# Optimization experiments

Measured on AMD Instinct MI355X. Metric: run time of the kernel, lower is better.

## Reference

```python
import jax, jax.numpy as jnp
import numpy as np

D_MODEL = 1024
NUM_HEADS = 16
D_K = D_MODEL // NUM_HEADS


def setup_inputs() -> dict:
    key = jax.random.key(0)
    ks = jax.random.split(key, 11)
    B, S, D = 2, 2048, D_MODEL
    s = 1.0 / np.sqrt(D)
    return {
        "Q": jax.random.normal(ks[0], (B, S, D), jnp.float32),
        "K": jax.random.normal(ks[1], (B, S, D), jnp.float32),
        "V": jax.random.normal(ks[2], (B, S, D), jnp.float32),
        "Wq": jax.random.normal(ks[3], (D, D), jnp.float32) * s,
        "bq": jax.random.normal(ks[4], (D,), jnp.float32) * s,
        "Wk": jax.random.normal(ks[5], (D, D), jnp.float32) * s,
        "bk": jax.random.normal(ks[6], (D,), jnp.float32) * s,
        "Wv": jax.random.normal(ks[7], (D, D), jnp.float32) * s,
        "bv": jax.random.normal(ks[8], (D,), jnp.float32) * s,
        "Wo": jax.random.normal(ks[9], (D, D), jnp.float32) * s,
        "bo": jax.random.normal(ks[10], (D,), jnp.float32) * s,
    }


def _split_heads(x):
    B, S, D = x.shape
    return x.reshape(B, S, NUM_HEADS, D_K).transpose(0, 2, 1, 3)  # [B,H,S,d_k]


def reference(Q, K, V, Wq, bq, Wk, bk, Wv, bv, Wo, bo):
    q = _split_heads(Q @ Wq + bq)
    k = _split_heads(K @ Wk + bk)
    v = _split_heads(V @ Wv + bv)
    scale = 1.0 / np.sqrt(D_K)
    scores = jnp.einsum('bhqd,bhkd->bhqk', q, k) * scale
    P = jax.nn.softmax(scores, axis=-1)  # max-subtract + exp + normalize
    O = jnp.einsum('bhqk,bhkd->bhqd', P, v)
    B, H, S, dk = O.shape
    O = O.transpose(0, 2, 1, 3).reshape(B, S, H * dk)
    return O @ Wo + bo
```

## Files before the change

kernel.cpp:

```cpp
#include <hip/hip_runtime.h>
#include <math.h>

#define S_LEN 2048
#define DMODEL 1024
#define NHEADS 16
#define DK 64

#define QSCALE 0.1803368801111244f

typedef __attribute__((ext_vector_type(8))) _Float16 f16x8;
typedef __attribute__((ext_vector_type(2))) __fp16 hf16x2;
typedef __attribute__((ext_vector_type(4))) float f32x4;

static __device__ __forceinline__ unsigned short f2h(float f) {
    _Float16 h = (_Float16)f;
    return __builtin_bit_cast(unsigned short, h);
}

static __device__ __forceinline__ unsigned pack2(float a, float b) {
    hf16x2 h = __builtin_amdgcn_cvt_pkrtz(a, b);
    return __builtin_bit_cast(unsigned, h);
}

static __device__ __forceinline__ void gload16(const void* g, void* l) {
    __builtin_amdgcn_global_load_lds(
        (const __attribute__((address_space(1))) void*)g,
        (__attribute__((address_space(3))) void*)l, 16, 0, 0);
}

__global__ __launch_bounds__(256)
void cvt_f16_kernel(const float* __restrict__ s0, const float* __restrict__ s1,
                    const float* __restrict__ s2, unsigned short* __restrict__ d)
{
    const int z = blockIdx.y;
    const float* src = z == 0 ? s0 : (z == 1 ? s1 : s2);
    unsigned short* dst = d + (size_t)z * 4194304;
    const int i = (blockIdx.x * 256 + threadIdx.x) * 8;
    float4 a = *reinterpret_cast<const float4*>(src + i);
    float4 b = *reinterpret_cast<const float4*>(src + i + 4);
    uint4 o;
    o.x = pack2(a.x, a.y);
    o.y = pack2(a.z, a.w);
    o.z = pack2(b.x, b.y);
    o.w = pack2(b.z, b.w);
    *reinterpret_cast<uint4*>(dst + i) = o;
}

__global__ __launch_bounds__(256)
void wprep_kernel(const float* __restrict__ w0, const float* __restrict__ w1,
                  const float* __restrict__ w2, const float* __restrict__ w3,
                  unsigned short* __restrict__ wt)
{
    __shared__ float tile[64][65];
    const int z = blockIdx.z;
    const float* W = z == 0 ? w0 : (z == 1 ? w1 : (z == 2 ? w2 : w3));
    unsigned short* Wt = wt + (size_t)z * 1048576;
    const int k0 = blockIdx.x * 64, n0 = blockIdx.y * 64;
    const int t = threadIdx.x;
    #pragma unroll
    for (int i = 0; i < 4; ++i) {
        int idx = i * 256 + t;
        int r = idx >> 4, c4 = (idx & 15) * 4;
        float4 v = *reinterpret_cast<const float4*>(W + (size_t)(k0 + r) * 1024 + n0 + c4);
        tile[r][c4 + 0] = v.x; tile[r][c4 + 1] = v.y;
        tile[r][c4 + 2] = v.z; tile[r][c4 + 3] = v.w;
    }
    __syncthreads();
    #pragma unroll
    for (int i = 0; i < 4; ++i) {
        int idx = i * 256 + t;
        int nr = idx >> 4, kc4 = (idx & 15) * 4;
        ushort4 h;
        h.x = f2h(tile[kc4 + 0][nr]); h.y = f2h(tile[kc4 + 1][nr]);
        h.z = f2h(tile[kc4 + 2][nr]); h.w = f2h(tile[kc4 + 3][nr]);
        *reinterpret_cast<ushort4*>(Wt + (size_t)(n0 + nr) * 1024 + k0 + kc4) = h;
    }
}

__global__ __launch_bounds__(512)
void gemm_mfma_kernel(const unsigned short* __restrict__ xh_base,
                      const unsigned short* __restrict__ wt_base,
                      const float* __restrict__ b0, const float* __restrict__ b1,
                      const float* __restrict__ b2,
                      void* __restrict__ dst_base, int mode_base)
{
    __shared__ char Als[16384];
    __shared__ char Bls[16384];

    const int z = blockIdx.z;
    const char* Ag = (const char*)(xh_base + (size_t)z * 4194304);
    const char* Bg = (const char*)(wt_base + (size_t)z * 1048576);
    const float* bias = z == 0 ? b0 : (z == 1 ? b1 : b2);
    const int mode = mode_base < 0 ? z : mode_base;

    const int tid = threadIdx.x;
    const int w = tid >> 6, l = tid & 63, a = l & 15, g = l >> 4;
    const int wm = w >> 2, wn = w & 3;
    const int bm = blockIdx.y * 128, bn = blockIdx.x * 128;

    const int srow = tid >> 3;
    const int sc8 = tid & 7;

    f32x4 acc[4][2] = {};

    for (int k0b = 0; k0b < 2048; k0b += 128) {
        #pragma unroll
        for (int it = 0; it < 2; ++it) {
            const int row = it * 64 + srow;
            const int gc = (sc8 << 4) ^ ((row & 7) << 4);
            gload16(Ag + (size_t)(bm + row) * 2048 + k0b + gc,
                    &Als[(size_t)(it * 512 + tid) * 16]);
            gload16(Bg + (size_t)(bn + row) * 2048 + k0b + gc,
                    &Bls[(size_t)(it * 512 + tid) * 16]);
        }
        __syncthreads();
        #pragma unroll
        for (int kc = 0; kc < 2; ++kc) {
            f16x8 af[4], bf[2];
            #pragma unroll
            for (int mi = 0; mi < 4; ++mi) {
                const int row = wm * 64 + 16 * mi + a;
                af[mi] = *reinterpret_cast<const f16x8*>(
                    &Als[row * 128 + ((kc * 64 + g * 16) ^ ((row & 7) << 4))]);
            }
            #pragma unroll
            for (int ni = 0; ni < 2; ++ni) {
                const int row = wn * 32 + 16 * ni + a;
                bf[ni] = *reinterpret_cast<const f16x8*>(
                    &Bls[row * 128 + ((kc * 64 + g * 16) ^ ((row & 7) << 4))]);
            }
            __builtin_amdgcn_s_setprio(1);
            #pragma unroll
            for (int mi = 0; mi < 4; ++mi)
                #pragma unroll
                for (int ni = 0; ni < 2; ++ni)
                    acc[mi][ni] = __builtin_amdgcn_mfma_f32_16x16x32_f16(
                        af[mi], bf[ni], acc[mi][ni], 0, 0, 0);
            __builtin_amdgcn_s_setprio(0);
        }
        __syncthreads();
    }

    void* mydst = (mode == 3) ? dst_base
                 : (void*)((unsigned short*)dst_base + (size_t)z * 4194304);

    #pragma unroll
    for (int ni = 0; ni < 2; ++ni) {
        const int n = bn + wn * 32 + 16 * ni + a;
        const float bv = bias[n];
        #pragma unroll
        for (int mi = 0; mi < 4; ++mi) {
            const int mbase = bm + wm * 64 + 16 * mi + g * 4;
            if (mode == 3) {
                float* o = (float*)mydst;
                #pragma unroll
                for (int r = 0; r < 4; ++r)
                    o[(size_t)(mbase + r) * 1024 + n] = acc[mi][ni][r] + bv;
            } else if (mode == 2) {
                unsigned short* o = (unsigned short*)mydst;
                const int b = mbase >> 11, s = mbase & (S_LEN - 1);
                const int h = n >> 6, d = n & (DK - 1);
                ushort4 st;
                st.x = f2h(acc[mi][ni][0] + bv);
                st.y = f2h(acc[mi][ni][1] + bv);
                st.z = f2h(acc[mi][ni][2] + bv);
                st.w = f2h(acc[mi][ni][3] + bv);
                *reinterpret_cast<ushort4*>(
                    o + ((size_t)((b * NHEADS + h) * DK + d)) * S_LEN + s) = st;
            } else {
                unsigned short* o = (unsigned short*)mydst;
                const float sc = (mode == 0) ? QSCALE : 1.0f;
                #pragma unroll
                for (int r = 0; r < 4; ++r) {
                    const int m = mbase + r;
                    const int b = m >> 11, s = m & (S_LEN - 1);
                    const int h = n >> 6, d = n & (DK - 1);
                    o[((size_t)((b * NHEADS + h) * S_LEN + s)) * DK + d] =
                        f2h((acc[mi][ni][r] + bv) * sc);
                }
            }
        }
    }
}

__global__ __launch_bounds__(512, 4)
void attn_mfma_kernel(const unsigned short* __restrict__ qb,
                      const unsigned short* __restrict__ kb,
                      const unsigned short* __restrict__ vt,
                      unsigned short* __restrict__ ob)
{
    __shared__ char Kls[2][8192];
    __shared__ char Vls[2][8192];
    __shared__ unsigned short Pl[8][32][72];

    const int tid = threadIdx.x;
    const int w = tid >> 6;
    const int p = w >> 2;
    const int wsub = w & 3;
    const int l = tid & 63;
    const int a = l & 15;
    const int g = l >> 4;
    const int bh = blockIdx.y;
    const int q0 = blockIdx.x * 128 + wsub * 32;

    const unsigned short* qhead = qb + (size_t)bh * S_LEN * DK;
    const char* khead = (const char*)(kb + (size_t)bh * S_LEN * DK);
    const char* vhead = (const char*)(vt + (size_t)bh * DK * S_LEN);

    f16x8 qf[2][2];
    #pragma unroll
    for (int j = 0; j < 2; ++j)
        #pragma unroll
        for (int c = 0; c < 2; ++c)
            qf[j][c] = *reinterpret_cast<const f16x8*>(
                qhead + (size_t)(q0 + 16 * j + a) * DK + 32 * c + 8 * g);

    f16x8 onesf;
    #pragma unroll
    for (int i = 0; i < 8; ++i) onesf[i] = (_Float16)1.f;

    f32x4 oacc[4][2] = {};
    f32x4 lacc[2] = {};
    float mrun[2] = {-INFINITY, -INFINITY};

    const int srow = tid >> 3;
    const int sgc = ((tid & 7) << 4) ^ ((srow & 7) << 4);

    #define STAGE1(t2)                                                          \
        do {                                                                    \
            gload16(khead + (size_t)((t2) * 64 + srow) * 128 + sgc,             \
                    &Kls[(t2) & 1][(size_t)w * 1024]);                          \
            gload16(vhead + (size_t)srow * 4096 + (size_t)(t2) * 128 + sgc,     \
                    &Vls[(t2) & 1][(size_t)w * 1024]);                          \
        } while (0)

    STAGE1(0);
    STAGE1(1);
    __syncthreads();

    for (int i = 0; i < 16; ++i) {
        f16x8 kf[2][4];
        #pragma unroll
        for (int c = 0; c < 2; ++c)
            #pragma unroll
            for (int T = 0; T < 4; ++T) {
                const int row = 16 * T + a;
                kf[c][T] = *reinterpret_cast<const f16x8*>(
                    &Kls[p][row * 128 + ((64 * c + 16 * g) ^ ((row & 7) << 4))]);
            }

        #pragma unroll
        for (int j = 0; j < 2; ++j) {
            f32x4 sacc[4] = {};
            __builtin_amdgcn_s_setprio(1);
            #pragma unroll
            for (int c = 0; c < 2; ++c)
                #pragma unroll
                for (int T = 0; T < 4; ++T)
                    sacc[T] = __builtin_amdgcn_mfma_f32_16x16x32_f16(
                        kf[c][T], qf[j][c], sacc[T], 0, 0, 0);
            __builtin_amdgcn_s_setprio(0);

            float lm = -INFINITY;
            #pragma unroll
            for (int T = 0; T < 4; ++T)
                #pragma unroll
                for (int r = 0; r < 4; ++r) lm = fmaxf(lm, sacc[T][r]);

            if (!__all(lm <= mrun[j] + 8.f)) {
                float vmax = fmaxf(lm, __shfl_xor(lm, 16));
                vmax = fmaxf(vmax, __shfl_xor(vmax, 32));
                const float mnew = fmaxf(mrun[j], vmax);
                const float corr = __builtin_amdgcn_exp2f(mrun[j] - mnew);
                #pragma unroll
                for (int t = 0; t < 4; ++t) {
                    oacc[t][j][0] *= corr; oacc[t][j][1] *= corr;
                    oacc[t][j][2] *= corr; oacc[t][j][3] *= corr;
                }
                lacc[j][0] *= corr; lacc[j][1] *= corr;
                lacc[j][2] *= corr; lacc[j][3] *= corr;
                mrun[j] = mnew;
            }

            const float mj = mrun[j];
            #pragma unroll
            for (int T = 0; T < 4; ++T) {
                float e0 = __builtin_amdgcn_exp2f(sacc[T][0] - mj);
                float e1 = __builtin_amdgcn_exp2f(sacc[T][1] - mj);
                float e2 = __builtin_amdgcn_exp2f(sacc[T][2] - mj);
                float e3 = __builtin_amdgcn_exp2f(sacc[T][3] - mj);
                unsigned* dst = reinterpret_cast<unsigned*>(
                    &Pl[w][16 * j + a][16 * T + 4 * g]);
                dst[0] = pack2(e0, e1);
                dst[1] = pack2(e2, e3);
            }
        }

        f16x8 vf[2][4];
        #pragma unroll
        for (int c = 0; c < 2; ++c)
            #pragma unroll
            for (int t = 0; t < 4; ++t) {
                const int row = 16 * t + a;
                vf[c][t] = *reinterpret_cast<const f16x8*>(
                    &Vls[p][row * 128 + ((64 * c + 16 * g) ^ ((row & 7) << 4))]);
            }

        __syncthreads();
        if (i < 15) {
            STAGE1(2 * i + 2);
            STAGE1(2 * i + 3);
        }

        #pragma unroll
        for (int c = 0; c < 2; ++c) {
            f16x8 pf[2];
            #pragma unroll
            for (int j = 0; j < 2; ++j)
                pf[j] = *reinterpret_cast<const f16x8*>(
                    &Pl[w][16 * j + a][32 * c + 8 * g]);
            __builtin_amdgcn_s_setprio(1);
            #pragma unroll
            for (int t = 0; t < 4; ++t)
                #pragma unroll
                for (int j = 0; j < 2; ++j)
                    oacc[t][j] = __builtin_amdgcn_mfma_f32_16x16x32_f16(
                        vf[c][t], pf[j], oacc[t][j], 0, 0, 0);
            #pragma unroll
            for (int j = 0; j < 2; ++j)
                lacc[j] = __builtin_amdgcn_mfma_f32_16x16x32_f16(
                    onesf, pf[j], lacc[j], 0, 0, 0);
            __builtin_amdgcn_s_setprio(0);
        }
        __syncthreads();
    }
    #undef STAGE1

    float* Ob = (float*)Pl;
    float* Ml = (float*)Kls;
    if (p == 1) {
        #pragma unroll
        for (int j = 0; j < 2; ++j) {
            if (g == 0) {
                Ml[((wsub * 2 + j) * 2 + 0) * 16 + a] = mrun[j];
                Ml[((wsub * 2 + j) * 2 + 1) * 16 + a] = lacc[j][0];
            }
            #pragma unroll
            for (int t = 0; t < 4; ++t)
                #pragma unroll
                for (int r = 0; r < 4; ++r)
                    Ob[((wsub * 2 + j) * 64 + 16 * t + 4 * g + r) * 16 + a] =
                        oacc[t][j][r];
        }
    }
    __syncthreads();
    if (p == 0) {
        const int b = bh >> 4;
        const int h = bh & (NHEADS - 1);
        #pragma unroll
        for (int j = 0; j < 2; ++j) {
            const float m1 = Ml[((wsub * 2 + j) * 2 + 0) * 16 + a];
            const float l1 = Ml[((wsub * 2 + j) * 2 + 1) * 16 + a];
            const float m0 = mrun[j];
            const float ms = fmaxf(m0, m1);
            const float c0 = __builtin_amdgcn_exp2f(m0 - ms);
            const float c1 = __builtin_amdgcn_exp2f(m1 - ms);
            const float inv = 1.f / (lacc[j][0] * c0 + l1 * c1);
            unsigned short* dst0 =
                ob + (size_t)(b * S_LEN + q0 + 16 * j + a) * DMODEL + h * DK;
            #pragma unroll
            for (int t = 0; t < 4; ++t) {
                ushort4 st;
                #pragma unroll
                for (int r = 0; r < 4; ++r) {
                    const float o1 =
                        Ob[((wsub * 2 + j) * 64 + 16 * t + 4 * g + r) * 16 + a];
                    const float val = (oacc[t][j][r] * c0 + o1 * c1) * inv;
                    ((unsigned short*)&st)[r] = f2h(val);
                }
                *reinterpret_cast<ushort4*>(dst0 + 16 * t + 4 * g) = st;
            }
        }
    }
}

extern "C" void kernel_launch(void* const* d_in, const int* in_sizes, int n_in,
                              void* d_out, int out_size, void* d_ws, size_t ws_size,
                              hipStream_t stream)
{
    const float* Q  = (const float*)d_in[0];
    const float* K  = (const float*)d_in[1];
    const float* V  = (const float*)d_in[2];
    const float* Wq = (const float*)d_in[3];
    const float* bq = (const float*)d_in[4];
    const float* Wk = (const float*)d_in[5];
    const float* bk = (const float*)d_in[6];
    const float* Wv = (const float*)d_in[7];
    const float* bv = (const float*)d_in[8];
    const float* Wo = (const float*)d_in[9];
    const float* bo = (const float*)d_in[10];
    float* out = (float*)d_out;

    unsigned short* xh  = (unsigned short*)d_ws;
    unsigned short* wt  = xh + (size_t)3 * 4194304;
    unsigned short* qb  = wt + (size_t)4 * 1048576;
    unsigned short* kb  = qb + 4194304;
    unsigned short* vtb = kb + 4194304;
    unsigned short* obh = vtb + 4194304;

    cvt_f16_kernel<<<dim3(2048, 3), 256, 0, stream>>>(Q, K, V, xh);
    wprep_kernel<<<dim3(16, 16, 4), 256, 0, stream>>>(Wq, Wk, Wv, Wo, wt);

    gemm_mfma_kernel<<<dim3(8, 32, 3), 512, 0, stream>>>(
        xh, wt, bq, bk, bv, qb, -1);

    attn_mfma_kernel<<<dim3(S_LEN / 128, 2 * NHEADS), 512, 0, stream>>>(qb, kb, vtb, obh);

    gemm_mfma_kernel<<<dim3(8, 32, 1), 512, 0, stream>>>(
        obh, wt + (size_t)3 * 1048576, bo, bo, bo, out, 3);
}
```

Baseline: 137.1 us.

## Fuse fp32-to-fp16 input conversion into projection GEMM A-tile loading

Drops the separate cvt_f16 pass over Q/K/V. The projection GEMM now reads fp32 activations directly into registers, packs them to fp16, and writes them into swizzled LDS. This removes one kernel launch and the write plus re-read of a 24 MB fp16 intermediate. In exchange, the A tile is re-read in fp32 by each of the 8 column blocks, doubling A-side global traffic in the GEMM, and the A loads now go through registers instead of async global-to-LDS loads.

```diff
diff --git a/kernel.cpp b/kernel.cpp
--- a/kernel.cpp
+++ b/kernel.cpp
@@ -26,24 +26,6 @@
     __builtin_amdgcn_global_load_lds(
         (const __attribute__((address_space(1))) void*)g,
         (__attribute__((address_space(3))) void*)l, 16, 0, 0);
-}
-
-__global__ __launch_bounds__(256)
-void cvt_f16_kernel(const float* __restrict__ s0, const float* __restrict__ s1,
-                    const float* __restrict__ s2, unsigned short* __restrict__ d)
-{
-    const int z = blockIdx.y;
-    const float* src = z == 0 ? s0 : (z == 1 ? s1 : s2);
-    unsigned short* dst = d + (size_t)z * 4194304;
-    const int i = (blockIdx.x * 256 + threadIdx.x) * 8;
-    float4 a = *reinterpret_cast<const float4*>(src + i);
-    float4 b = *reinterpret_cast<const float4*>(src + i + 4);
-    uint4 o;
-    o.x = pack2(a.x, a.y);
-    o.y = pack2(a.z, a.w);
-    o.z = pack2(b.x, b.y);
-    o.w = pack2(b.z, b.w);
-    *reinterpret_cast<uint4*>(dst + i) = o;
 }
 
 __global__ __launch_bounds__(256)
@@ -78,41 +60,60 @@
 }
 
 __global__ __launch_bounds__(512)
-void gemm_mfma_kernel(const unsigned short* __restrict__ xh_base,
+void proj_gemm_kernel(const float* __restrict__ x0, const float* __restrict__ x1,
+                      const float* __restrict__ x2,
                       const unsigned short* __restrict__ wt_base,
                       const float* __restrict__ b0, const float* __restrict__ b1,
                       const float* __restrict__ b2,
-                      void* __restrict__ dst_base, int mode_base)
+                      unsigned short* __restrict__ dst_base)
 {
     __shared__ char Als[16384];
     __shared__ char Bls[16384];
 
     const int z = blockIdx.z;
-    const char* Ag = (const char*)(xh_base + (size_t)z * 4194304);
+    const float* Ag = z == 0 ? x0 : (z == 1 ? x1 : x2);
     const char* Bg = (const char*)(wt_base + (size_t)z * 1048576);
     const float* bias = z == 0 ? b0 : (z == 1 ? b1 : b2);
-    const int mode = mode_base < 0 ? z : mode_base;
+    const int mode = z;
 
     const int tid = threadIdx.x;
     const int w = tid >> 6, l = tid & 63, a = l & 15, g = l >> 4;
     const int wm = w >> 2, wn = w & 3;
     const int bm = blockIdx.y * 128, bn = blockIdx.x * 128;
 
+    const int arow = tid >> 2;
+    const int ac16 = tid & 3;
+    const int aswz = (arow & 7) << 4;
     const int srow = tid >> 3;
     const int sc8 = tid & 7;
 
     f32x4 acc[4][2] = {};
 
-    for (int k0b = 0; k0b < 2048; k0b += 128) {
+    for (int ks = 0; ks < 16; ++ks) {
+        const float* ap = Ag + (size_t)(bm + arow) * 1024 + ks * 64 + 16 * ac16;
+        float4 a0 = reinterpret_cast<const float4*>(ap)[0];
+        float4 a1 = reinterpret_cast<const float4*>(ap)[1];
+        float4 a2 = reinterpret_cast<const float4*>(ap)[2];
+        float4 a3 = reinterpret_cast<const float4*>(ap)[3];
+
         #pragma unroll
         for (int it = 0; it < 2; ++it) {
             const int row = it * 64 + srow;
             const int gc = (sc8 << 4) ^ ((row & 7) << 4);
-            gload16(Ag + (size_t)(bm + row) * 2048 + k0b + gc,
-                    &Als[(size_t)(it * 512 + tid) * 16]);
-            gload16(Bg + (size_t)(bn + row) * 2048 + k0b + gc,
+            gload16(Bg + (size_t)(bn + row) * 2048 + ks * 128 + gc,
                     &Bls[(size_t)(it * 512 + tid) * 16]);
         }
+
+        uint4 w0, w1;
+        w0.x = pack2(a0.x, a0.y); w0.y = pack2(a0.z, a0.w);
+        w0.z = pack2(a1.x, a1.y); w0.w = pack2(a1.z, a1.w);
+        w1.x = pack2(a2.x, a2.y); w1.y = pack2(a2.z, a2.w);
+        w1.z = pack2(a3.x, a3.y); w1.w = pack2(a3.z, a3.w);
+        const int abase = arow * 128;
+        const int aoff = 32 * ac16;
+        *reinterpret_cast<uint4*>(&Als[abase + (aoff ^ aswz)]) = w0;
+        *reinterpret_cast<uint4*>(&Als[abase + ((aoff + 16) ^ aswz)]) = w1;
+
         __syncthreads();
         #pragma unroll
         for (int kc = 0; kc < 2; ++kc) {
@@ -141,8 +142,7 @@
         __syncthreads();
     }
 
-    void* mydst = (mode == 3) ? dst_base
-                 : (void*)((unsigned short*)dst_base + (size_t)z * 4194304);
+    unsigned short* mydst = dst_base + (size_t)z * 4194304;
 
     #pragma unroll
     for (int ni = 0; ni < 2; ++ni) {
@@ -151,13 +151,7 @@
         #pragma unroll
         for (int mi = 0; mi < 4; ++mi) {
             const int mbase = bm + wm * 64 + 16 * mi + g * 4;
-            if (mode == 3) {
-                float* o = (float*)mydst;
-                #pragma unroll
-                for (int r = 0; r < 4; ++r)
-                    o[(size_t)(mbase + r) * 1024 + n] = acc[mi][ni][r] + bv;
-            } else if (mode == 2) {
-                unsigned short* o = (unsigned short*)mydst;
+            if (mode == 2) {
                 const int b = mbase >> 11, s = mbase & (S_LEN - 1);
                 const int h = n >> 6, d = n & (DK - 1);
                 ushort4 st;
@@ -166,19 +160,91 @@
                 st.z = f2h(acc[mi][ni][2] + bv);
                 st.w = f2h(acc[mi][ni][3] + bv);
                 *reinterpret_cast<ushort4*>(
-                    o + ((size_t)((b * NHEADS + h) * DK + d)) * S_LEN + s) = st;
+                    mydst + ((size_t)((b * NHEADS + h) * DK + d)) * S_LEN + s) = st;
             } else {
-                unsigned short* o = (unsigned short*)mydst;
                 const float sc = (mode == 0) ? QSCALE : 1.0f;
                 #pragma unroll
                 for (int r = 0; r < 4; ++r) {
                     const int m = mbase + r;
                     const int b = m >> 11, s = m & (S_LEN - 1);
                     const int h = n >> 6, d = n & (DK - 1);
-                    o[((size_t)((b * NHEADS + h) * S_LEN + s)) * DK + d] =
+                    mydst[((size_t)((b * NHEADS + h) * S_LEN + s)) * DK + d] =
                         f2h((acc[mi][ni][r] + bv) * sc);
                 }
             }
+        }
+    }
+}
+
+__global__ __launch_bounds__(512)
+void out_gemm_kernel(const unsigned short* __restrict__ Agh,
+                     const unsigned short* __restrict__ Bgh,
+                     const float* __restrict__ bias, float* __restrict__ out)
+{
+    __shared__ char Als[16384];
+    __shared__ char Bls[16384];
+
+    const char* Ag = (const char*)Agh;
+    const char* Bg = (const char*)Bgh;
+
+    const int tid = threadIdx.x;
+    const int w = tid >> 6, l = tid & 63, a = l & 15, g = l >> 4;
+    const int wm = w >> 2, wn = w & 3;
+    const int bm = blockIdx.y * 128, bn = blockIdx.x * 128;
+
+    const int srow = tid >> 3;
+    const int sc8 = tid & 7;
+
+    f32x4 acc[4][2] = {};
+
+    for (int k0b = 0; k0b < 2048; k0b += 128) {
+        #pragma unroll
+        for (int it = 0; it < 2; ++it) {
+            const int row = it * 64 + srow;
+            const int gc = (sc8 << 4) ^ ((row & 7) << 4);
+            gload16(Ag + (size_t)(bm + row) * 2048 + k0b + gc,
+                    &Als[(size_t)(it * 512 + tid) * 16]);
+            gload16(Bg + (size_t)(bn + row) * 2048 + k0b + gc,
+                    &Bls[(size_t)(it * 512 + tid) * 16]);
+        }
+        __syncthreads();
+        #pragma unroll
+        for (int kc = 0; kc < 2; ++kc) {
+            f16x8 af[4], bf[2];
+            #pragma unroll
+            for (int mi = 0; mi < 4; ++mi) {
+                const int row = wm * 64 + 16 * mi + a;
+                af[mi] = *reinterpret_cast<const f16x8*>(
+                    &Als[row * 128 + ((kc * 64 + g * 16) ^ ((row & 7) << 4))]);
+            }
+            #pragma unroll
+            for (int ni = 0; ni < 2; ++ni) {
+                const int row = wn * 32 + 16 * ni + a;
+                bf[ni] = *reinterpret_cast<const f16x8*>(
+                    &Bls[row * 128 + ((kc * 64 + g * 16) ^ ((row & 7) << 4))]);
+            }
+            __builtin_amdgcn_s_setprio(1);
+            #pragma unroll
+            for (int mi = 0; mi < 4; ++mi)
+                #pragma unroll
+                for (int ni = 0; ni < 2; ++ni)
+                    acc[mi][ni] = __builtin_amdgcn_mfma_f32_16x16x32_f16(
+                        af[mi], bf[ni], acc[mi][ni], 0, 0, 0);
+            __builtin_amdgcn_s_setprio(0);
+        }
+        __syncthreads();
+    }
+
+    #pragma unroll
+    for (int ni = 0; ni < 2; ++ni) {
+        const int n = bn + wn * 32 + 16 * ni + a;
+        const float bv = bias[n];
+        #pragma unroll
+        for (int mi = 0; mi < 4; ++mi) {
+            const int mbase = bm + wm * 64 + 16 * mi + g * 4;
+            #pragma unroll
+            for (int r = 0; r < 4; ++r)
+                out[(size_t)(mbase + r) * 1024 + n] = acc[mi][ni][r] + bv;
         }
     }
 }
@@ -408,14 +474,13 @@
     unsigned short* vtb = kb + 4194304;
     unsigned short* obh = vtb + 4194304;
 
-    cvt_f16_kernel<<<dim3(2048, 3), 256, 0, stream>>>(Q, K, V, xh);
     wprep_kernel<<<dim3(16, 16, 4), 256, 0, stream>>>(Wq, Wk, Wv, Wo, wt);
 
-    gemm_mfma_kernel<<<dim3(8, 32, 3), 512, 0, stream>>>(
-        xh, wt, bq, bk, bv, qb, -1);
+    proj_gemm_kernel<<<dim3(8, 32, 3), 512, 0, stream>>>(
+        Q, K, V, wt, bq, bk, bv, qb);
 
     attn_mfma_kernel<<<dim3(S_LEN / 128, 2 * NHEADS), 512, 0, stream>>>(qb, kb, vtb, obh);
 
-    gemm_mfma_kernel<<<dim3(8, 32, 1), 512, 0, stream>>>(
-        obh, wt + (size_t)3 * 1048576, bo, bo, bo, out, 3);
-}
+    out_gemm_kernel<<<dim3(8, 32, 1), 512, 0, stream>>>(
+        obh, wt + (size_t)3 * 1048576, bo, out);
+}
```

Measured after the change: 144.8 us. +5.6%, slower.
